# Performance work log

Measured on AMD Instinct MI355X. Metric: run time of the kernel, lower is better.

Reference implementation:

```python
import jax, jax.numpy as jnp
import numpy as np

N, E, De, Dv = 40000, 8000, 32, 8   # nodes, hyperedges, edge degree, node degree
D, Q, EIG, VOC, NC = 256, 256, 64, 1000, 40  # vertex/edge dim, query dim, eig dim, centrality vocab, classes
LN_EPS = 1e-5


def _linear(x, W, b):
    return x @ W + b


def _layernorm(x, g, b):
    mu = jnp.mean(x, axis=-1, keepdims=True)
    var = jnp.mean(jnp.square(x - mu), axis=-1, keepdims=True)
    return (x - mu) * jax.lax.rsqrt(var + LN_EPS) * g + b


def setup_inputs() -> dict:
    key = jax.random.key(0)
    ks = iter(jax.random.split(key, 64))
    def nrm(shape, s=0.02):
        return (jax.random.normal(next(ks), shape, jnp.float32) * s).astype(jnp.float32)
    inp = {
        'vfeat': jax.random.normal(next(ks), (N, D), jnp.float32),
        'efeat': jax.random.normal(next(ks), (E, D), jnp.float32),
        'eign_vec': jax.random.normal(next(ks), (N, EIG), jnp.float32),
        'feat_v_gcn': jax.random.normal(next(ks), (N, D), jnp.float32),
        'cent1': jax.random.uniform(next(ks), (E, De), jnp.float32),
        'cent2': jax.random.uniform(next(ks), (N, Dv), jnp.float32),
        'cent_idx': jax.random.randint(next(ks), (N,), 0, VOC),
        'uniq_idx': jax.random.randint(next(ks), (N,), 0, VOC),
        'edge2node': jax.random.randint(next(ks), (E, De), 0, N),
        'node2edge': jax.random.randint(next(ks), (N, Dv), 0, E),
        # learned parameters (W: [in, out])
        'W_vtx': nrm((D, D)), 'b_vtx': jnp.zeros((D,), jnp.float32),
        'W_pe': nrm((EIG, D)), 'b_pe': jnp.zeros((D,), jnp.float32),
        'cs_emb': nrm((VOC, D)), 'un_emb': nrm((VOC, D)),
        'W_kv': nrm((D, Q)), 'b_kv': jnp.zeros((Q,), jnp.float32),
        'W_vv': nrm((D, D)), 'b_vv': jnp.zeros((D,), jnp.float32),
        'W_qe': nrm((D, Q)), 'b_qe': jnp.zeros((Q,), jnp.float32),
        'W_ke': nrm((D, Q)), 'b_ke': jnp.zeros((Q,), jnp.float32),
        'W_ve': nrm((D, D)), 'b_ve': jnp.zeros((D,), jnp.float32),
        'W_qv': nrm((D, Q)), 'b_qv': jnp.zeros((Q,), jnp.float32),
        'W_l1': nrm((D, Q)), 'b_l1': jnp.zeros((Q,), jnp.float32),
        'W_l2': nrm((Q, D)), 'b_l2': jnp.zeros((D,), jnp.float32),
        'W_l3': nrm((D, Q)), 'b_l3': jnp.zeros((Q,), jnp.float32),
        'W_l4': nrm((Q, D)), 'b_l4': jnp.zeros((D,), jnp.float32),
        'ln1_g': jnp.ones((D,), jnp.float32), 'ln1_b': jnp.zeros((D,), jnp.float32),
        'ln2_g': jnp.ones((D,), jnp.float32), 'ln2_b': jnp.zeros((D,), jnp.float32),
        'W_cls': nrm((D, NC)), 'b_cls': jnp.zeros((NC,), jnp.float32),
    }
    return inp


def _forward(vfeat, efeat, eign_vec, feat_v_gcn, cent1, cent2,
             W_vtx, b_vtx, W_pe, b_pe, cs_emb, un_emb,
             W_kv, b_kv, W_vv, b_vv, W_qe, b_qe, W_ke, b_ke, W_ve, b_ve, W_qv, b_qv,
             W_l1, b_l1, W_l2, b_l2, W_l3, b_l3, W_l4, b_l4,
             ln1_g, ln1_b, ln2_g, ln2_b, W_cls, b_cls,
             cent_idx, uniq_idx, edge2node, node2edge):
    scale = 1.0 / np.sqrt(float(W_kv.shape[1]))  # 1/sqrt(query_dim)
    # first_layer feature assembly: vtx_lin_1layer + PE + GCN + centrality/uniqueness embeddings
    feat_v = (_linear(vfeat, W_vtx, b_vtx) + _linear(eign_vec, W_pe, b_pe)
              + feat_v_gcn + cs_emb[cent_idx] + un_emb[uniq_idx])
    feat_e = efeat

    # ---- stage 1: hyperedges attend over member nodes ('in' etype) ----
    k_n = _linear(feat_v, W_kv, b_kv)              # [N,Q]
    v_n = _linear(feat_v, W_vv, b_vv)              # [N,D]
    q_e = _linear(feat_e, W_qe, b_qe)              # [E,Q]
    km = k_n[edge2node]                            # [E,De,Q]
    attn = jax.nn.leaky_relu(jnp.einsum('edq,eq->ed', km, q_e), 0.01) * scale
    score = jax.nn.softmax(attn + cent1, axis=1)   # centrality-biased softmax (k-core + clustering)
    h_e = jnp.einsum('ed,edc->ec', score, v_n[edge2node])  # [E,D]
    x_e = _layernorm(h_e + feat_e, ln1_g, ln1_b)
    f_e = _linear(jax.nn.relu(_linear(x_e, W_l1, b_l1)), W_l2, b_l2)
    feat_e = _layernorm(f_e + x_e, ln1_g, ln1_b)

    # ---- stage 2: nodes attend over incident hyperedges ('con' etype) ----
    k_e = _linear(feat_e, W_ke, b_ke)              # [E,Q]
    v_e = _linear(feat_e, W_ve, b_ve)              # [E,D]
    q_v = _linear(feat_v, W_qv, b_qv)              # [N,Q]
    km2 = k_e[node2edge]                           # [N,Dv,Q]
    attn2 = jax.nn.leaky_relu(jnp.einsum('ndq,nq->nd', km2, q_v), 0.01) * scale
    score2 = jax.nn.softmax(attn2 + cent2, axis=1)
    h_v = jnp.einsum('nd,ndc->nc', score2, v_e[node2edge])  # [N,D]
    x_v = _layernorm(h_v + feat_v, ln2_g, ln2_b)
    f_v = _linear(jax.nn.relu(_linear(x_v, W_l3, b_l3)), W_l4, b_l4)
    feat_v = _layernorm(f_v + x_v, ln2_g, ln2_b)

    # last_layer classification head (dropout is identity in eval)
    return _linear(feat_v, W_cls, b_cls)           # [N,NC]


def reference(vfeat, efeat, eign_vec, feat_v_gcn, cent1, cent2,
              cent_idx, uniq_idx, edge2node, node2edge,
              W_vtx, b_vtx, W_pe, b_pe, cs_emb, un_emb,
              W_kv, b_kv, W_vv, b_vv, W_qe, b_qe, W_ke, b_ke, W_ve, b_ve, W_qv, b_qv,
              W_l1, b_l1, W_l2, b_l2, W_l3, b_l3, W_l4, b_l4,
              ln1_g, ln1_b, ln2_g, ln2_b, W_cls, b_cls):
    return _forward(vfeat, efeat, eign_vec, feat_v_gcn, cent1, cent2,
                    W_vtx, b_vtx, W_pe, b_pe, cs_emb, un_emb,
                    W_kv, b_kv, W_vv, b_vv, W_qe, b_qe, W_ke, b_ke, W_ve, b_ve, W_qv, b_qv,
                    W_l1, b_l1, W_l2, b_l2, W_l3, b_l3, W_l4, b_l4,
                    ln1_g, ln1_b, ln2_g, ln2_b, W_cls, b_cls,
                    cent_idx, uniq_idx, edge2node, node2edge)
```

## Files before the change

### kernel.cpp

```cpp
#include <hip/hip_runtime.h>
#include <hip/hip_bf16.h>
#include <cstddef>

#define N_NODES 40000
#define N_EDGES 8000
#define DE 32
#define DV 8
#define DIM 256
#define QDIM 256
#define EIGD 64
#define NCLS 40
#define LN_EPS 1e-5f
#define ATT_SCALE 0.0625f

typedef unsigned short u16;
typedef unsigned int u32;
using i16x8 = __attribute__((ext_vector_type(8))) short;
using f32x4 = __attribute__((ext_vector_type(4))) float;

__device__ inline u16 f2b(float f) {
    union { float f; u32 u; } c; c.f = f;
    u32 u = c.u + 0x7FFF + ((c.u >> 16) & 1);
    return (u16)(u >> 16);
}
__device__ inline float b2f(u16 b) {
    union { u32 u; float f; } c; c.u = (u32)b << 16;
    return c.f;
}

__device__ inline void gload_lds16(const u16* g, u16* l) {
    __builtin_amdgcn_global_load_lds(
        (const __attribute__((address_space(1))) void*)g,
        (__attribute__((address_space(3))) void*)l, 16, 0, 0);
}

#define VMCNT12 asm volatile("s_waitcnt vmcnt(12)" ::: "memory")
#define VMCNT6  asm volatile("s_waitcnt vmcnt(6)" ::: "memory")
#define VMCNT5  asm volatile("s_waitcnt vmcnt(5)" ::: "memory")
#define VMCNT4  asm volatile("s_waitcnt vmcnt(4)" ::: "memory")
#define VMCNT0  asm volatile("s_waitcnt vmcnt(0)" ::: "memory")
#define LGKM0   asm volatile("s_waitcnt lgkmcnt(0)" ::: "memory")

__global__ __launch_bounds__(256) void prep_weights(
    const float* w0, const float* w1, const float* w2, const float* w3,
    const float* w4, const float* w5, const float* w6, const float* w7,
    const float* w8, const float* w9, const float* w10, const float* w11,
    const float* w12, u16* __restrict__ pool)
{
    const float* srcs[13] = {w0,w1,w2,w3,w4,w5,w6,w7,w8,w9,w10,w11,w12};
    const int Ks[13]  = {256,64,256,256,256,256,256,256,256,256,256,256,256};
    const int Nds[13] = {256,256,256,256,256,256,256,256,256,256,256,256,40};
    const int id = blockIdx.z;
    const float* W = srcs[id];
    u16* Wt = pool + (size_t)id * 65536;
    const int K = Ks[id], Nd = Nds[id];
    const int k0 = blockIdx.x * 32, n0 = blockIdx.y * 32;
    if (k0 >= K || n0 >= Nd) return;

    __shared__ float tile[32][33];
    const int x = threadIdx.x & 31, y4 = (threadIdx.x >> 5) * 4;
#pragma unroll
    for (int j = 0; j < 4; j++) {
        int k = k0 + y4 + j;
        tile[y4 + j][x] = (k < K && (n0 + x) < Nd) ? W[(size_t)k * Nd + n0 + x] : 0.f;
    }
    __syncthreads();
#pragma unroll
    for (int j = 0; j < 4; j++) {
        int n = n0 + y4 + j;
        if (n < Nd && (k0 + x) < K)
            Wt[(size_t)n * K + k0 + x] = f2b(tile[x][y4 + j]);
    }
}

#define MST 264
__global__ __launch_bounds__(256, 2) void asm_kvq(
    const float* __restrict__ vfeat, const float* __restrict__ eign,
    const u16* __restrict__ Wt_vtx, const u16* __restrict__ Wt_pe,
    const float* __restrict__ b_vtx, const float* __restrict__ b_pe,
    const float* __restrict__ gcn, const float* __restrict__ emb1,
    const float* __restrict__ emb2, const int* __restrict__ idx1,
    const int* __restrict__ idx2,
    const u16* __restrict__ Wt_kvq, const float* __restrict__ b_kv,
    const float* __restrict__ b_vv, const float* __restrict__ b_qv,
    u16* __restrict__ FVb, u16* __restrict__ KVQn)
{
    __shared__ __align__(16) u16 Asm[2][64 * 32];
    __shared__ __align__(16) u16 Bsm[2][256 * 32];
    __shared__ __align__(16) u16 Msm[64 * MST];
    const int t = threadIdx.x;
    const int lane = t & 63, w = t >> 6;
    const int row0 = blockIdx.x * 64;

    const int srow = lane >> 2;
    const int sblk = ((lane & 3) ^ ((lane >> 3) & 3)) * 8;
    const int fr = lane & 15, h = lane >> 4;
    const int rsw = (fr >> 1) & 3;

    f32x4 acc[4][4] = {};
    float4 fA[2][2];

    auto p1_issueB = [&](int kt) {
        const int buf = kt & 1;
        const int k0 = kt << 5;
        const bool tail = (k0 >= 256);
#pragma unroll
        for (int i = 0; i < 4; i++) {
            const int r = w * 64 + i * 16;
            const u16* gp = tail ? Wt_pe + (size_t)(r + srow) * 64 + (k0 - 256) + sblk
                                 : Wt_vtx + (size_t)(r + srow) * 256 + k0 + sblk;
            gload_lds16(gp, &Bsm[buf][r * 32]);
        }
    };
    auto p1_loadA = [&](int kt) {
        const int k0 = kt << 5;
        const bool tail = (k0 >= 256);
        const float* ap = tail
            ? eign + (size_t)(row0 + w * 16 + srow) * 64 + (k0 - 256) + sblk
            : vfeat + (size_t)(row0 + w * 16 + srow) * 256 + k0 + sblk;
        fA[kt & 1][0] = *(const float4*)ap;
        fA[kt & 1][1] = *(const float4*)(ap + 4);
    };
    auto p1_write = [&](int kt) {
        const int buf = kt & 1;
        float4 f0 = fA[buf][0], f1 = fA[buf][1];
        i16x8 v;
        v[0] = (short)f2b(f0.x); v[1] = (short)f2b(f0.y);
        v[2] = (short)f2b(f0.z); v[3] = (short)f2b(f0.w);
        v[4] = (short)f2b(f1.x); v[5] = (short)f2b(f1.y);
        v[6] = (short)f2b(f1.z); v[7] = (short)f2b(f1.w);
        *(i16x8*)&Asm[buf][(w * 16 + srow) * 32 + (lane & 3) * 8] = v;
    };

    p1_loadA(0); p1_issueB(0); p1_loadA(1); p1_write(0);
#pragma unroll
    for (int kt = 0; kt < 10; ++kt) {
        const int buf = kt & 1;
        if (kt + 1 < 10) p1_issueB(kt + 1);
        if (kt + 2 < 10) p1_loadA(kt + 2);
        if (kt + 1 < 10) p1_write(kt + 1);
        else { VMCNT0; }
        LGKM0;
        __builtin_amdgcn_s_barrier();

        i16x8 af[4], bfr[4];
#pragma unroll
        for (int m = 0; m < 4; m++)
            af[m] = *(const i16x8*)&Asm[buf][(m * 16 + fr) * 32 + (h ^ rsw) * 8];
#pragma unroll
        for (int n = 0; n < 4; n++)
            bfr[n] = *(const i16x8*)&Bsm[buf][(w * 64 + n * 16 + fr) * 32 + (h ^ rsw) * 8];
        LGKM0;
        __builtin_amdgcn_sched_barrier(0);
        __builtin_amdgcn_s_barrier();

#pragma unroll
        for (int m = 0; m < 4; m++)
#pragma unroll
            for (int n = 0; n < 4; n++)
                acc[m][n] = __builtin_amdgcn_mfma_f32_16x16x32_bf16(
                    af[m], bfr[n], acc[m][n], 0, 0, 0);
    }

#pragma unroll
    for (int m = 0; m < 4; m++)
#pragma unroll
        for (int j = 0; j < 4; j++) {
            const int row = m * 16 + h * 4 + j;
#pragma unroll
            for (int n = 0; n < 4; n++) {
                const int col = w * 64 + n * 16 + fr;
                float v = acc[m][n][j] + b_vtx[col] + b_pe[col];
                Msm[row * MST + col] = f2b(v);
                acc[m][n][j] = 0.f;
            }
        }
    __syncthreads();

    const float4* gcn4 = (const float4*)gcn;
    const float4* e1_4 = (const float4*)emb1;
    const float4* e2_4 = (const float4*)emb2;
    ushort4* FVb4 = (ushort4*)FVb;
#pragma unroll 4
    for (int it = 0; it < 16; ++it) {
        const int T = t + it * 256;
        const int row = T >> 6, cg = T & 63;
        const int grow = row0 + row;
        const int i1 = idx1[grow], i2 = idx2[grow];
        ushort4 mv = *(const ushort4*)&Msm[row * MST + cg * 4];
        float4 gv = gcn4[(size_t)grow * 64 + cg];
        float4 e1 = e1_4[(size_t)i1 * 64 + cg];
        float4 e2 = e2_4[(size_t)i2 * 64 + cg];
        ushort4 o;
        o.x = f2b(b2f(mv.x) + gv.x + e1.x + e2.x);
        o.y = f2b(b2f(mv.y) + gv.y + e1.y + e2.y);
        o.z = f2b(b2f(mv.z) + gv.z + e1.z + e2.z);
        o.w = f2b(b2f(mv.w) + gv.w + e1.w + e2.w);
        FVb4[(size_t)grow * 64 + cg] = o;
        *(ushort4*)&Msm[row * MST + cg * 4] = o;
    }
    __syncthreads();

    auto p2_issueB = [&](int buf, int kt, const u16* Wb) {
#pragma unroll
        for (int i = 0; i < 4; i++) {
            const int r = w * 64 + i * 16;
            gload_lds16(Wb + (size_t)(r + srow) * 256 + (kt << 5) + sblk,
                        &Bsm[buf][r * 32]);
        }
    };
#pragma unroll 1
    for (int c = 0; c < 3; ++c) {
        const u16* Wb = Wt_kvq + (size_t)c * 256 * 256;
        const float* bc = (c == 0) ? b_kv : ((c == 1) ? b_vv : b_qv);
#pragma unroll
        for (int m = 0; m < 4; m++)
#pragma unroll
            for (int n = 0; n < 4; n++)
                acc[m][n] = f32x4{0.f, 0.f, 0.f, 0.f};
        p2_issueB(0, 0, Wb);
#pragma unroll
        for (int kt = 0; kt < 8; ++kt) {
            const int buf = kt & 1;
            if (kt < 7) { p2_issueB(buf ^ 1, kt + 1, Wb); VMCNT4; }
            else { VMCNT0; }
            __builtin_amdgcn_s_barrier();

            i16x8 af[4], bfr[4];
#pragma unroll
            for (int m = 0; m < 4; m++)
                af[m] = *(const i16x8*)&Msm[(m * 16 + fr) * MST + (kt << 5) + h * 8];
#pragma unroll
            for (int n = 0; n < 4; n++)
                bfr[n] = *(const i16x8*)&Bsm[buf][(w * 64 + n * 16 + fr) * 32 + (h ^ rsw) * 8];
            LGKM0;
            __builtin_amdgcn_sched_barrier(0);
            __builtin_amdgcn_s_barrier();

#pragma unroll
            for (int m = 0; m < 4; m++)
#pragma unroll
                for (int n = 0; n < 4; n++)
                    acc[m][n] = __builtin_amdgcn_mfma_f32_16x16x32_bf16(
                        af[m], bfr[n], acc[m][n], 0, 0, 0);
        }
#pragma unroll
        for (int m = 0; m < 4; m++)
#pragma unroll
            for (int j = 0; j < 4; j++) {
                const int grow = row0 + m * 16 + h * 4 + j;
#pragma unroll
                for (int n = 0; n < 4; n++) {
                    const int gcol = w * 64 + n * 16 + fr;
                    KVQn[(size_t)grow * 768 + c * 256 + gcol] =
                        f2b(acc[m][n][j] + bc[gcol]);
                }
            }
    }
}

template <int EPI, int AMODE, int NT>
__global__ __launch_bounds__(256, 2) void gemmN(
    const void* __restrict__ Av, const u16* __restrict__ Wt,
    const float* __restrict__ bias0, const float* __restrict__ bias1,
    const float* __restrict__ bias2,
    void* __restrict__ Cv, int Nd)
{
    __shared__ u16 Asm[3][64 * 64];
    __shared__ u16 Bsm[3][128 * 64];
    const int t = threadIdx.x;
    const int lane = t & 63, w = t >> 6;
    const int wr = w >> 1, wc = w & 1;
    const int row0 = blockIdx.y * 64, col0 = blockIdx.x * 128;

    f32x4 acc[2][4] = {};

    const int srow = lane >> 3;
    const int sblk = ((lane & 7) ^ srow) * 8;
    const int fr = lane & 15, h = lane >> 4;
    const int lsw = fr & 7;

    float4 farA[2][2][2];

    auto stage_load = [&](int kt) {
        const int buf = kt % 3;
        const int k0 = kt << 6;
        if constexpr (AMODE == 0) {
#pragma unroll
            for (int i = 0; i < 2; i++) {
                const int r = w * 16 + i * 8;
                gload_lds16((const u16*)Av + (size_t)(row0 + r + srow) * 256 + k0 + sblk,
                            &Asm[buf][r * 64]);
            }
        } else {
#pragma unroll
            for (int i = 0; i < 2; i++) {
                const int r = w * 16 + i * 8;
                const float* ap = (const float*)Av + (size_t)(row0 + r + srow) * 256 + k0 + sblk;
                farA[kt & 1][i][0] = *(const float4*)ap;
                farA[kt & 1][i][1] = *(const float4*)(ap + 4);
            }
        }
#pragma unroll
        for (int i = 0; i < 4; i++) {
            const int r = w * 32 + i * 8;
            int ng = col0 + r + srow; if (ng > Nd - 1) ng = Nd - 1;
            gload_lds16(Wt + (size_t)ng * 256 + k0 + sblk, &Bsm[buf][r * 64]);
        }
    };
    auto stage_write = [&](int kt) {
        const int buf = kt % 3;
#pragma unroll
        for (int i = 0; i < 2; i++) {
            const int r = w * 16 + i * 8;
            float4 f0 = farA[kt & 1][i][0], f1 = farA[kt & 1][i][1];
            i16x8 v;
            v[0] = (short)f2b(f0.x); v[1] = (short)f2b(f0.y);
            v[2] = (short)f2b(f0.z); v[3] = (short)f2b(f0.w);
            v[4] = (short)f2b(f1.x); v[5] = (short)f2b(f1.y);
            v[6] = (short)f2b(f1.z); v[7] = (short)f2b(f1.w);
            *(i16x8*)&Asm[buf][(r + srow) * 64 + (lane & 7) * 8] = v;
        }
    };

    stage_load(0);
    if (NT > 1) stage_load(1);
    if constexpr (AMODE != 0) stage_write(0);

#pragma unroll
    for (int kt = 0; kt < NT; ++kt) {
        const int buf = kt % 3;
        if (kt + 2 < NT) stage_load(kt + 2);
        if constexpr (AMODE != 0) {
            if (kt + 1 < NT) stage_write(kt + 1);
            else { VMCNT0; }
        } else {
            if (kt + 2 < NT) { VMCNT12; }
            else if (kt + 1 < NT) { VMCNT6; }
            else { VMCNT0; }
        }
        LGKM0;
        __builtin_amdgcn_s_barrier();

        i16x8 af[2][2], bfr[2][4];
#pragma unroll
        for (int kk = 0; kk < 2; kk++) {
#pragma unroll
            for (int m = 0; m < 2; m++)
                af[kk][m] = *(const i16x8*)&Asm[buf][(wr * 32 + m * 16 + fr) * 64 +
                                                    ((kk * 4 + h) ^ lsw) * 8];
#pragma unroll
            for (int n = 0; n < 4; n++)
                bfr[kk][n] = *(const i16x8*)&Bsm[buf][(wc * 64 + n * 16 + fr) * 64 +
                                                     ((kk * 4 + h) ^ lsw) * 8];
        }
        LGKM0;
        __builtin_amdgcn_sched_barrier(0);
        __builtin_amdgcn_s_barrier();

#pragma unroll
        for (int kk = 0; kk < 2; kk++)
#pragma unroll
            for (int m = 0; m < 2; m++)
#pragma unroll
                for (int n = 0; n < 4; n++)
                    acc[m][n] = __builtin_amdgcn_mfma_f32_16x16x32_bf16(
                        af[kk][m], bfr[kk][n], acc[m][n], 0, 0, 0);
    }

    const int seg = (int)(blockIdx.x >> 1);
    const float* bp = (seg == 0) ? bias0 : ((seg == 1) ? bias1 : bias2);
#pragma unroll
    for (int m = 0; m < 2; m++) {
#pragma unroll
        for (int j = 0; j < 4; j++) {
            const int grow = row0 + wr * 32 + m * 16 + h * 4 + j;
#pragma unroll
            for (int n = 0; n < 4; n++) {
                const int gcol = col0 + wc * 64 + n * 16 + fr;
                if (EPI == 4 && gcol >= Nd) continue;
                float v = acc[m][n][j] + bp[gcol & 255];
                if constexpr (EPI == 1) v = fmaxf(v, 0.f);
                if constexpr (EPI == 4)
                    ((float*)Cv)[(size_t)grow * Nd + gcol] = v;
                else
                    ((u16*)Cv)[(size_t)grow * Nd + gcol] = f2b(v);
            }
        }
    }
}

template <int TAIL>
__global__ __launch_bounds__(256, 2) void ffn_fused(
    const u16* __restrict__ X, const u16* __restrict__ Wt1,
    const float* __restrict__ b1, const u16* __restrict__ Wt2,
    const float* __restrict__ b2, const float* __restrict__ lng,
    const float* __restrict__ lnb, const u16* __restrict__ WtT,
    const float* __restrict__ bT0, const float* __restrict__ bT1,
    void* __restrict__ outp)
{
    __shared__ __align__(16) u16 Asm[2][64 * 32];
    __shared__ __align__(16) u16 Bsm[2][256 * 32];
    __shared__ __align__(16) u16 Msm[64 * MST];
    const int t = threadIdx.x;
    const int lane = t & 63, w = t >> 6;
    const int row0 = blockIdx.x * 64;

    const int srow = lane >> 2;
    const int sblk = ((lane & 3) ^ ((lane >> 3) & 3)) * 8;
    const int fr = lane & 15, h = lane >> 4;
    const int rsw = (fr >> 1) & 3;

    f32x4 acc[4][4] = {};

    auto stageA = [&](int buf, int kt) {
        gload_lds16(X + (size_t)(row0 + w * 16 + srow) * 256 + (kt << 5) + sblk,
                    &Asm[buf][(w * 16) * 32]);
    };
    auto stageB = [&](int buf, int kt, const u16* W) {
#pragma unroll
        for (int i = 0; i < 4; i++) {
            const int r = w * 64 + i * 16;
            gload_lds16(W + (size_t)(r + srow) * 256 + (kt << 5) + sblk,
                        &Bsm[buf][r * 32]);
        }
    };

    stageA(0, 0); stageB(0, 0, Wt1);
#pragma unroll
    for (int kt = 0; kt < 8; ++kt) {
        const int buf = kt & 1;
        if (kt < 7) { stageA(buf ^ 1, kt + 1); stageB(buf ^ 1, kt + 1, Wt1); VMCNT5; }
        else { VMCNT0; }
        __builtin_amdgcn_s_barrier();

        i16x8 af[4], bfr[4];
#pragma unroll
        for (int m = 0; m < 4; m++)
            af[m] = *(const i16x8*)&Asm[buf][(m * 16 + fr) * 32 + (h ^ rsw) * 8];
#pragma unroll
        for (int n = 0; n < 4; n++)
            bfr[n] = *(const i16x8*)&Bsm[buf][(w * 64 + n * 16 + fr) * 32 + (h ^ rsw) * 8];
        LGKM0;
        __builtin_amdgcn_sched_barrier(0);
        __builtin_amdgcn_s_barrier();

#pragma unroll
        for (int m = 0; m < 4; m++)
#pragma unroll
            for (int n = 0; n < 4; n++)
                acc[m][n] = __builtin_amdgcn_mfma_f32_16x16x32_bf16(
                    af[m], bfr[n], acc[m][n], 0, 0, 0);
    }
    {
        float b1v[4];
#pragma unroll
        for (int n = 0; n < 4; n++) b1v[n] = b1[w * 64 + n * 16 + fr];
#pragma unroll
        for (int m = 0; m < 4; m++)
#pragma unroll
            for (int j = 0; j < 4; j++) {
                const int row = m * 16 + h * 4 + j;
#pragma unroll
                for (int n = 0; n < 4; n++) {
                    const int col = w * 64 + n * 16 + fr;
                    float v = fmaxf(acc[m][n][j] + b1v[n], 0.f);
                    Msm[row * MST + col] = f2b(v);
                    acc[m][n][j] = 0.f;
                }
            }
    }
    __syncthreads();

    stageB(0, 0, Wt2);
#pragma unroll
    for (int kt = 0; kt < 8; ++kt) {
        const int buf = kt & 1;
        if (kt < 7) { stageB(buf ^ 1, kt + 1, Wt2); VMCNT4; }
        else { VMCNT0; }
        __builtin_amdgcn_s_barrier();

        i16x8 af[4], bfr[4];
#pragma unroll
        for (int m = 0; m < 4; m++)
            af[m] = *(const i16x8*)&Msm[(m * 16 + fr) * MST + (kt << 5) + h * 8];
#pragma unroll
        for (int n = 0; n < 4; n++)
            bfr[n] = *(const i16x8*)&Bsm[buf][(w * 64 + n * 16 + fr) * 32 + (h ^ rsw) * 8];
        LGKM0;
        __builtin_amdgcn_sched_barrier(0);
        __builtin_amdgcn_s_barrier();

#pragma unroll
        for (int m = 0; m < 4; m++)
#pragma unroll
            for (int n = 0; n < 4; n++)
                acc[m][n] = __builtin_amdgcn_mfma_f32_16x16x32_bf16(
                    af[m], bfr[n], acc[m][n], 0, 0, 0);
    }
    {
        float* redS = (float*)&Asm[0][0];
        float* redQ = redS + 256;
#pragma unroll
        for (int m = 0; m < 4; m++) {
#pragma unroll
            for (int j = 0; j < 4; j++) {
                const int grow = row0 + m * 16 + h * 4 + j;
                float s = 0.f, q = 0.f;
#pragma unroll
                for (int n = 0; n < 4; n++) {
                    const int gcol = w * 64 + n * 16 + fr;
                    float v = acc[m][n][j] + b2[gcol] +
                              b2f(X[(size_t)grow * 256 + gcol]);
                    acc[m][n][j] = v;
                    s += v; q += v * v;
                }
#pragma unroll
                for (int off = 1; off < 16; off <<= 1) {
                    s += __shfl_xor(s, off, 64);
                    q += __shfl_xor(q, off, 64);
                }
                if (fr == 0) {
                    redS[(m * 16 + h * 4 + j) * 4 + w] = s;
                    redQ[(m * 16 + h * 4 + j) * 4 + w] = q;
                }
            }
        }
        __syncthreads();
#pragma unroll
        for (int m = 0; m < 4; m++) {
#pragma unroll
            for (int j = 0; j < 4; j++) {
                const int r = m * 16 + h * 4 + j;
                float4 s4 = *(const float4*)&redS[r * 4];
                float4 q4 = *(const float4*)&redQ[r * 4];
                float mu = (s4.x + s4.y + s4.z + s4.w) * (1.f / DIM);
                float var = (q4.x + q4.y + q4.z + q4.w) * (1.f / DIM) - mu * mu;
                float rr = rsqrtf(var + LN_EPS);
#pragma unroll
                for (int n = 0; n < 4; n++) {
                    const int gcol = w * 64 + n * 16 + fr;
                    float y = (acc[m][n][j] - mu) * rr * lng[gcol] + lnb[gcol];
                    acc[m][n][j] = y;
                }
            }
        }
        __syncthreads();
#pragma unroll
        for (int m = 0; m < 4; m++)
#pragma unroll
            for (int j = 0; j < 4; j++) {
                const int row = m * 16 + h * 4 + j;
#pragma unroll
                for (int n = 0; n < 4; n++)
                    Msm[row * MST + (w * 64 + n * 16 + fr)] = f2b(acc[m][n][j]);
            }
    }
    VMCNT0;
    __syncthreads();

    if constexpr (TAIL == 0) {
        u16* KVe = (u16*)outp;
#pragma unroll
        for (int half = 0; half < 2; half++) {
            const u16* Wb = WtT + (size_t)half * 256 * 256;
            const float* bT = half ? bT1 : bT0;
#pragma unroll
            for (int m = 0; m < 4; m++)
#pragma unroll
                for (int n = 0; n < 4; n++)
                    acc[m][n] = f32x4{0.f, 0.f, 0.f, 0.f};
            stageB(0, 0, Wb);
#pragma unroll
            for (int kt = 0; kt < 8; ++kt) {
                const int buf = kt & 1;
                if (kt < 7) { stageB(buf ^ 1, kt + 1, Wb); VMCNT4; }
                else { VMCNT0; }
                __builtin_amdgcn_s_barrier();

                i16x8 af[4], bfr[4];
#pragma unroll
                for (int m = 0; m < 4; m++)
                    af[m] = *(const i16x8*)&Msm[(m * 16 + fr) * MST + (kt << 5) + h * 8];
#pragma unroll
                for (int n = 0; n < 4; n++)
                    bfr[n] = *(const i16x8*)&Bsm[buf][(w * 64 + n * 16 + fr) * 32 + (h ^ rsw) * 8];
                LGKM0;
                __builtin_amdgcn_sched_barrier(0);
                __builtin_amdgcn_s_barrier();

#pragma unroll
                for (int m = 0; m < 4; m++)
#pragma unroll
                    for (int n = 0; n < 4; n++)
                        acc[m][n] = __builtin_amdgcn_mfma_f32_16x16x32_bf16(
                            af[m], bfr[n], acc[m][n], 0, 0, 0);
            }
#pragma unroll
            for (int m = 0; m < 4; m++)
#pragma unroll
                for (int j = 0; j < 4; j++) {
                    const int grow = row0 + m * 16 + h * 4 + j;
#pragma unroll
                    for (int n = 0; n < 4; n++) {
                        const int gcol = w * 64 + n * 16 + fr;
                        KVe[(size_t)grow * 512 + half * 256 + gcol] =
                            f2b(acc[m][n][j] + bT[gcol]);
                    }
                }
        }
    } else {
        float* out = (float*)outp;
        f32x4 acc3[3] = {};
#pragma unroll
        for (int kk = 0; kk < 8; kk++) {
            i16x8 af = *(const i16x8*)&Msm[(w * 16 + fr) * MST + kk * 32 + h * 8];
#pragma unroll
            for (int n = 0; n < 3; n++) {
                int br = n * 16 + fr; if (br > NCLS - 1) br = NCLS - 1;
                i16x8 bfr = *(const i16x8*)(WtT + (size_t)br * 256 + kk * 32 + h * 8);
                acc3[n] = __builtin_amdgcn_mfma_f32_16x16x32_bf16(af, bfr, acc3[n], 0, 0, 0);
            }
        }
#pragma unroll
        for (int n = 0; n < 3; n++) {
            const int gcol = n * 16 + fr;
            if (gcol >= NCLS) continue;
#pragma unroll
            for (int j = 0; j < 4; j++) {
                const int grow = row0 + w * 16 + h * 4 + j;
                out[(size_t)grow * NCLS + gcol] = acc3[n][j] + bT0[gcol];
            }
        }
    }
}

__global__ __launch_bounds__(256) void edge_attn(
    const u16* __restrict__ KVQn, const u16* __restrict__ QE,
    const float* __restrict__ efeat,
    const int* __restrict__ e2n, const float* __restrict__ cent1,
    const float* __restrict__ g, const float* __restrict__ bb,
    u16* __restrict__ XE)
{
    const int lane = threadIdx.x & 63, w = threadIdx.x >> 6;
    const int e = blockIdx.x * 4 + w;
    const int c4 = lane * 4;

    ushort4 q4 = *(const ushort4*)&QE[(size_t)e * QDIM + c4];
    const float q0 = b2f(q4.x), q1 = b2f(q4.y), q2 = b2f(q4.z), q3 = b2f(q4.w);

    int4 rv[8];
#pragma unroll
    for (int i = 0; i < 8; i++)
        rv[i] = *(const int4*)&e2n[(size_t)e * DE + i * 4];
    int rows[DE];
#pragma unroll
    for (int i = 0; i < 8; i++) {
        rows[i * 4 + 0] = rv[i].x; rows[i * 4 + 1] = rv[i].y;
        rows[i * 4 + 2] = rv[i].z; rows[i * 4 + 3] = rv[i].w;
    }

    float p[DE];
#pragma unroll
    for (int g0 = 0; g0 < DE; g0 += 16) {
        ushort4 k4[16];
#pragma unroll
        for (int j = 0; j < 16; j++)
            k4[j] = *(const ushort4*)&KVQn[(size_t)rows[g0 + j] * 768 + c4];
#pragma unroll
        for (int j = 0; j < 16; j++)
            p[g0 + j] = q0 * b2f(k4[j].x) + q1 * b2f(k4[j].y)
                      + q2 * b2f(k4[j].z) + q3 * b2f(k4[j].w);
    }
#pragma unroll
    for (int off = 32; off; off >>= 1)
#pragma unroll
        for (int d = 0; d < DE; d++)
            p[d] += __shfl_xor(p[d], off, 64);

    float4 cv[8];
#pragma unroll
    for (int i = 0; i < 8; i++)
        cv[i] = *(const float4*)&cent1[(size_t)e * DE + i * 4];
    float cent[DE];
#pragma unroll
    for (int i = 0; i < 8; i++) {
        cent[i * 4 + 0] = cv[i].x; cent[i * 4 + 1] = cv[i].y;
        cent[i * 4 + 2] = cv[i].z; cent[i * 4 + 3] = cv[i].w;
    }
#pragma unroll
    for (int d = 0; d < DE; d++)
        p[d] = (p[d] > 0.f ? p[d] : 0.01f * p[d]) * ATT_SCALE + cent[d];

    float mx = p[0];
#pragma unroll
    for (int d = 1; d < DE; d++) mx = fmaxf(mx, p[d]);
    float s = 0.f;
#pragma unroll
    for (int d = 0; d < DE; d++) { p[d] = __expf(p[d] - mx); s += p[d]; }
    const float inv = 1.f / s;
#pragma unroll
    for (int d = 0; d < DE; d++) p[d] *= inv;

    float a0 = 0.f, a1 = 0.f, a2 = 0.f, a3 = 0.f;
#pragma unroll
    for (int g0 = 0; g0 < DE; g0 += 16) {
        ushort4 v4[16];
#pragma unroll
        for (int j = 0; j < 16; j++)
            v4[j] = *(const ushort4*)&KVQn[(size_t)rows[g0 + j] * 768 + 256 + c4];
#pragma unroll
        for (int j = 0; j < 16; j++) {
            const float sd = p[g0 + j];
            a0 = fmaf(sd, b2f(v4[j].x), a0); a1 = fmaf(sd, b2f(v4[j].y), a1);
            a2 = fmaf(sd, b2f(v4[j].z), a2); a3 = fmaf(sd, b2f(v4[j].w), a3);
        }
    }
    float4 ef = *(const float4*)&efeat[(size_t)e * DIM + c4];
    float x0 = a0 + ef.x, x1 = a1 + ef.y, x2 = a2 + ef.z, x3 = a3 + ef.w;

    float mu = x0 + x1 + x2 + x3;
#pragma unroll
    for (int off = 32; off; off >>= 1) mu += __shfl_xor(mu, off, 64);
    mu *= (1.f / DIM);
    float d0 = x0 - mu, d1 = x1 - mu, d2 = x2 - mu, d3 = x3 - mu;
    float var = d0 * d0 + d1 * d1 + d2 * d2 + d3 * d3;
#pragma unroll
    for (int off = 32; off; off >>= 1) var += __shfl_xor(var, off, 64);
    var *= (1.f / DIM);
    float r = rsqrtf(var + LN_EPS);
    float4 gv = *(const float4*)&g[c4];
    float4 bv = *(const float4*)&bb[c4];
    ushort4 o;
    o.x = f2b(d0 * r * gv.x + bv.x); o.y = f2b(d1 * r * gv.y + bv.y);
    o.z = f2b(d2 * r * gv.z + bv.z); o.w = f2b(d3 * r * gv.w + bv.w);
    *(ushort4*)&XE[(size_t)e * DIM + c4] = o;
}

__global__ __launch_bounds__(256) void node_attn(
    const u16* __restrict__ KVe, const u16* __restrict__ KVQn,
    const u16* __restrict__ FV,
    const int* __restrict__ n2e, const float* __restrict__ cent2,
    const float* __restrict__ g, const float* __restrict__ bb,
    u16* __restrict__ XV)
{
    const int lane = threadIdx.x & 63, w = threadIdx.x >> 6;
    const int na = blockIdx.x * 8 + w * 2, nb = na + 1;
    const int c4 = lane * 4;

    ushort4 qa4 = *(const ushort4*)&KVQn[(size_t)na * 768 + 512 + c4];
    ushort4 qb4 = *(const ushort4*)&KVQn[(size_t)nb * 768 + 512 + c4];
    const float qa0 = b2f(qa4.x), qa1 = b2f(qa4.y), qa2 = b2f(qa4.z), qa3 = b2f(qa4.w);
    const float qb0 = b2f(qb4.x), qb1 = b2f(qb4.y), qb2 = b2f(qb4.z), qb3 = b2f(qb4.w);

    int4 r0 = *(const int4*)&n2e[(size_t)na * DV];
    int4 r1 = *(const int4*)&n2e[(size_t)na * DV + 4];
    int4 r2 = *(const int4*)&n2e[(size_t)nb * DV];
    int4 r3 = *(const int4*)&n2e[(size_t)nb * DV + 4];
    int rA[8] = {r0.x, r0.y, r0.z, r0.w, r1.x, r1.y, r1.z, r1.w};
    int rB[8] = {r2.x, r2.y, r2.z, r2.w, r3.x, r3.y, r3.z, r3.w};

    ushort4 kA[8], vA[8], kB[8], vB[8];
#pragma unroll
    for (int d = 0; d < DV; d++) {
        const u16* b = KVe + (size_t)rA[d] * 512 + c4;
        kA[d] = *(const ushort4*)b; vA[d] = *(const ushort4*)(b + 256);
    }
#pragma unroll
    for (int d = 0; d < DV; d++) {
        const u16* b = KVe + (size_t)rB[d] * 512 + c4;
        kB[d] = *(const ushort4*)b; vB[d] = *(const ushort4*)(b + 256);
    }

    float pA[8], pB[8];
#pragma unroll
    for (int d = 0; d < DV; d++) {
        pA[d] = qa0 * b2f(kA[d].x) + qa1 * b2f(kA[d].y)
              + qa2 * b2f(kA[d].z) + qa3 * b2f(kA[d].w);
        pB[d] = qb0 * b2f(kB[d].x) + qb1 * b2f(kB[d].y)
              + qb2 * b2f(kB[d].z) + qb3 * b2f(kB[d].w);
    }
#pragma unroll
    for (int off = 32; off; off >>= 1) {
#pragma unroll
        for (int d = 0; d < DV; d++) {
            pA[d] += __shfl_xor(pA[d], off, 64);
            pB[d] += __shfl_xor(pB[d], off, 64);
        }
    }
    float4 cA0 = *(const float4*)&cent2[(size_t)na * DV];
    float4 cA1 = *(const float4*)&cent2[(size_t)na * DV + 4];
    float4 cB0 = *(const float4*)&cent2[(size_t)nb * DV];
    float4 cB1 = *(const float4*)&cent2[(size_t)nb * DV + 4];
    float cA[8] = {cA0.x, cA0.y, cA0.z, cA0.w, cA1.x, cA1.y, cA1.z, cA1.w};
    float cB[8] = {cB0.x, cB0.y, cB0.z, cB0.w, cB1.x, cB1.y, cB1.z, cB1.w};
#pragma unroll
    for (int d = 0; d < DV; d++) {
        pA[d] = (pA[d] > 0.f ? pA[d] : 0.01f * pA[d]) * ATT_SCALE + cA[d];
        pB[d] = (pB[d] > 0.f ? pB[d] : 0.01f * pB[d]) * ATT_SCALE + cB[d];
    }
    float mA = pA[0], mB = pB[0];
#pragma unroll
    for (int d = 1; d < DV; d++) { mA = fmaxf(mA, pA[d]); mB = fmaxf(mB, pB[d]); }
    float sA = 0.f, sB = 0.f;
#pragma unroll
    for (int d = 0; d < DV; d++) {
        pA[d] = __expf(pA[d] - mA); sA += pA[d];
        pB[d] = __expf(pB[d] - mB); sB += pB[d];
    }
    const float iA = 1.f / sA, iB = 1.f / sB;

    float a0 = 0.f, a1 = 0.f, a2 = 0.f, a3 = 0.f;
    float b0 = 0.f, b1 = 0.f, b2 = 0.f, b3 = 0.f;
#pragma unroll
    for (int d = 0; d < DV; d++) {
        const float sa = pA[d] * iA, sb = pB[d] * iB;
        a0 = fmaf(sa, b2f(vA[d].x), a0); a1 = fmaf(sa, b2f(vA[d].y), a1);
        a2 = fmaf(sa, b2f(vA[d].z), a2); a3 = fmaf(sa, b2f(vA[d].w), a3);
        b0 = fmaf(sb, b2f(vB[d].x), b0); b1 = fmaf(sb, b2f(vB[d].y), b1);
        b2 = fmaf(sb, b2f(vB[d].z), b2); b3 = fmaf(sb, b2f(vB[d].w), b3);
    }
    ushort4 fa = *(const ushort4*)&FV[(size_t)na * DIM + c4];
    ushort4 fb = *(const ushort4*)&FV[(size_t)nb * DIM + c4];
    float xa0 = a0 + b2f(fa.x), xa1 = a1 + b2f(fa.y);
    float xa2 = a2 + b2f(fa.z), xa3 = a3 + b2f(fa.w);
    float xb0 = b0 + b2f(fb.x), xb1 = b1 + b2f(fb.y);
    float xb2 = b2 + b2f(fb.z), xb3 = b3 + b2f(fb.w);

    float muA = xa0 + xa1 + xa2 + xa3, muB = xb0 + xb1 + xb2 + xb3;
#pragma unroll
    for (int off = 32; off; off >>= 1) {
        muA += __shfl_xor(muA, off, 64);
        muB += __shfl_xor(muB, off, 64);
    }
    muA *= (1.f / DIM); muB *= (1.f / DIM);
    float da0 = xa0 - muA, da1 = xa1 - muA, da2 = xa2 - muA, da3 = xa3 - muA;
    float db0 = xb0 - muB, db1 = xb1 - muB, db2 = xb2 - muB, db3 = xb3 - muB;
    float vA_ = da0 * da0 + da1 * da1 + da2 * da2 + da3 * da3;
    float vB_ = db0 * db0 + db1 * db1 + db2 * db2 + db3 * db3;
#pragma unroll
    for (int off = 32; off; off >>= 1) {
        vA_ += __shfl_xor(vA_, off, 64);
        vB_ += __shfl_xor(vB_, off, 64);
    }
    const float rA_ = rsqrtf(vA_ * (1.f / DIM) + LN_EPS);
    const float rB_ = rsqrtf(vB_ * (1.f / DIM) + LN_EPS);
    float4 gv = *(const float4*)&g[c4];
    float4 bv = *(const float4*)&bb[c4];
    ushort4 oa, ob;
    oa.x = f2b(da0 * rA_ * gv.x + bv.x); oa.y = f2b(da1 * rA_ * gv.y + bv.y);
    oa.z = f2b(da2 * rA_ * gv.z + bv.z); oa.w = f2b(da3 * rA_ * gv.w + bv.w);
    ob.x = f2b(db0 * rB_ * gv.x + bv.x); ob.y = f2b(db1 * rB_ * gv.y + bv.y);
    ob.z = f2b(db2 * rB_ * gv.z + bv.z); ob.w = f2b(db3 * rB_ * gv.w + bv.w);
    *(ushort4*)&XV[(size_t)na * DIM + c4] = oa;
    *(ushort4*)&XV[(size_t)nb * DIM + c4] = ob;
}

extern "C" void kernel_launch(void* const* d_in, const int* in_sizes, int n_in,
                              void* d_out, int out_size, void* d_ws, size_t ws_size,
                              hipStream_t stream)
{
    const float* vfeat  = (const float*)d_in[0];
    const float* efeat  = (const float*)d_in[1];
    const float* eign   = (const float*)d_in[2];
    const float* gcn    = (const float*)d_in[3];
    const float* cent1  = (const float*)d_in[4];
    const float* cent2  = (const float*)d_in[5];
    const int*   cidx   = (const int*)d_in[6];
    const int*   uidx   = (const int*)d_in[7];
    const int*   e2n    = (const int*)d_in[8];
    const int*   n2e    = (const int*)d_in[9];
    const float* W_vtx  = (const float*)d_in[10]; const float* b_vtx = (const float*)d_in[11];
    const float* W_pe   = (const float*)d_in[12]; const float* b_pe  = (const float*)d_in[13];
    const float* cs_emb = (const float*)d_in[14]; const float* un_emb= (const float*)d_in[15];
    const float* W_kv   = (const float*)d_in[16]; const float* b_kv  = (const float*)d_in[17];
    const float* W_vv   = (const float*)d_in[18]; const float* b_vv  = (const float*)d_in[19];
    const float* W_qe   = (const float*)d_in[20]; const float* b_qe  = (const float*)d_in[21];
    const float* W_ke   = (const float*)d_in[22]; const float* b_ke  = (const float*)d_in[23];
    const float* W_ve   = (const float*)d_in[24]; const float* b_ve  = (const float*)d_in[25];
    const float* W_qv   = (const float*)d_in[26]; const float* b_qv  = (const float*)d_in[27];
    const float* W_l1   = (const float*)d_in[28]; const float* b_l1  = (const float*)d_in[29];
    const float* W_l2   = (const float*)d_in[30]; const float* b_l2  = (const float*)d_in[31];
    const float* W_l3   = (const float*)d_in[32]; const float* b_l3  = (const float*)d_in[33];
    const float* W_l4   = (const float*)d_in[34]; const float* b_l4  = (const float*)d_in[35];
    const float* ln1_g  = (const float*)d_in[36]; const float* ln1_b = (const float*)d_in[37];
    const float* ln2_g  = (const float*)d_in[38]; const float* ln2_b = (const float*)d_in[39];
    const float* W_cls  = (const float*)d_in[40]; const float* b_cls = (const float*)d_in[41];
    float* out = (float*)d_out;

    const size_t NE = (size_t)N_NODES * DIM;
    const size_t EE = (size_t)N_EDGES * DIM;
    u16* ws = (u16*)d_ws;
    u16* FVb  = ws;
    u16* KVQn = FVb + NE;
    u16* B2   = KVQn + 3 * NE;
    u16* QEb  = B2 + NE;
    u16* XE   = QEb + EE;
    u16* KVe  = XE + EE;
    u16* Wp   = KVe + 2 * EE;
    u16* Wt_vtx = Wp +  0 * 65536;
    u16* Wt_pe  = Wp +  1 * 65536;
    u16* Wt_kvq = Wp +  2 * 65536;
    u16* Wt_qe  = Wp +  5 * 65536;
    u16* Wt_kve = Wp +  6 * 65536;
    u16* Wt_l1  = Wp +  8 * 65536;
    u16* Wt_l2  = Wp +  9 * 65536;
    u16* Wt_l3  = Wp + 10 * 65536;
    u16* Wt_l4  = Wp + 11 * 65536;
    u16* Wt_cls = Wp + 12 * 65536;

    const dim3 blk(256);
    const dim3 gW(8, 8, 13);
    const dim3 gQE(2, N_EDGES / 64);

    prep_weights<<<gW, blk, 0, stream>>>(
        W_vtx, W_pe, W_kv, W_vv, W_qv, W_qe, W_ke, W_ve,
        W_l1, W_l2, W_l3, W_l4, W_cls, Wp);

    asm_kvq<<<N_NODES / 64, blk, 0, stream>>>(
        vfeat, eign, Wt_vtx, Wt_pe, b_vtx, b_pe,
        gcn, cs_emb, un_emb, cidx, uidx,
        Wt_kvq, b_kv, b_vv, b_qv, FVb, KVQn);

    gemmN<0, 1, 4><<<gQE, blk, 0, stream>>>(efeat, Wt_qe,
        b_qe, b_qe, b_qe, QEb, 256);
    edge_attn<<<N_EDGES / 4, blk, 0, stream>>>(KVQn, QEb, efeat, e2n, cent1,
        ln1_g, ln1_b, XE);
    ffn_fused<0><<<N_EDGES / 64, blk, 0, stream>>>(XE, Wt_l1, b_l1,
        Wt_l2, b_l2, ln1_g, ln1_b, Wt_kve, b_ke, b_ve, KVe);

    node_attn<<<N_NODES / 8, blk, 0, stream>>>(KVe, KVQn, FVb, n2e, cent2,
        ln2_g, ln2_b, B2);
    ffn_fused<1><<<N_NODES / 64, blk, 0, stream>>>(B2, Wt_l3, b_l3,
        Wt_l4, b_l4, ln2_g, ln2_b, Wt_cls, b_cls, nullptr, out);
}
```

Measured before the change: 237.3 us.

## Restructure LDS double-buffer pipeline to one barrier per k-step and prefetch across GEMMs

The double-buffered weight staging loops now issue the next tile's loads before the MFMA block and wait for them with a single vmcnt(0) plus barrier after compute, replacing the previous wait-then-barrier and second barrier before compute. The first tile of each following GEMM (next weight chunk, the second FFN weight, the tail weights) is prefetched during the last k-step of the current one, so there is no cold load between chained GEMMs. The aim is fewer barriers per iteration and overlap of global-to-LDS copies with MFMA work. The cost is a full vmcnt(0) drain each step and tighter reliance on barrier placement to avoid overwriting buffers still being read.

```diff
diff --git a/kernel.cpp b/kernel.cpp
--- a/kernel.cpp
+++ b/kernel.cpp
@@ -36,10 +36,10 @@
 
 #define VMCNT12 asm volatile("s_waitcnt vmcnt(12)" ::: "memory")
 #define VMCNT6  asm volatile("s_waitcnt vmcnt(6)" ::: "memory")
-#define VMCNT5  asm volatile("s_waitcnt vmcnt(5)" ::: "memory")
-#define VMCNT4  asm volatile("s_waitcnt vmcnt(4)" ::: "memory")
 #define VMCNT0  asm volatile("s_waitcnt vmcnt(0)" ::: "memory")
 #define LGKM0   asm volatile("s_waitcnt lgkmcnt(0)" ::: "memory")
+#define SCHED0  __builtin_amdgcn_sched_barrier(0)
+#define SBAR    __builtin_amdgcn_s_barrier()
 
 __global__ __launch_bounds__(256) void prep_weights(
     const float* w0, const float* w1, const float* w2, const float* w3,
@@ -141,7 +141,7 @@
         if (kt + 1 < 10) p1_write(kt + 1);
         else { VMCNT0; }
         LGKM0;
-        __builtin_amdgcn_s_barrier();
+        SBAR;
 
         i16x8 af[4], bfr[4];
 #pragma unroll
@@ -151,8 +151,8 @@
         for (int n = 0; n < 4; n++)
             bfr[n] = *(const i16x8*)&Bsm[buf][(w * 64 + n * 16 + fr) * 32 + (h ^ rsw) * 8];
         LGKM0;
-        __builtin_amdgcn_sched_barrier(0);
-        __builtin_amdgcn_s_barrier();
+        SCHED0;
+        SBAR;
 
 #pragma unroll
         for (int m = 0; m < 4; m++)
@@ -209,22 +209,22 @@
                         &Bsm[buf][r * 32]);
         }
     };
+    p2_issueB(0, 0, Wt_kvq);
+    VMCNT0; SBAR;
 #pragma unroll 1
     for (int c = 0; c < 3; ++c) {
-        const u16* Wb = Wt_kvq + (size_t)c * 256 * 256;
+        const u16* Wb = Wt_kvq + (size_t)c * 65536;
         const float* bc = (c == 0) ? b_kv : ((c == 1) ? b_vv : b_qv);
 #pragma unroll
         for (int m = 0; m < 4; m++)
 #pragma unroll
             for (int n = 0; n < 4; n++)
                 acc[m][n] = f32x4{0.f, 0.f, 0.f, 0.f};
-        p2_issueB(0, 0, Wb);
 #pragma unroll
         for (int kt = 0; kt < 8; ++kt) {
             const int buf = kt & 1;
-            if (kt < 7) { p2_issueB(buf ^ 1, kt + 1, Wb); VMCNT4; }
-            else { VMCNT0; }
-            __builtin_amdgcn_s_barrier();
+            if (kt < 7) p2_issueB(buf ^ 1, kt + 1, Wb);
+            else if (c < 2) p2_issueB(0, 0, Wb + 65536);
 
             i16x8 af[4], bfr[4];
 #pragma unroll
@@ -234,15 +234,14 @@
             for (int n = 0; n < 4; n++)
                 bfr[n] = *(const i16x8*)&Bsm[buf][(w * 64 + n * 16 + fr) * 32 + (h ^ rsw) * 8];
             LGKM0;
-            __builtin_amdgcn_sched_barrier(0);
-            __builtin_amdgcn_s_barrier();
-
+            SCHED0;
 #pragma unroll
             for (int m = 0; m < 4; m++)
 #pragma unroll
                 for (int n = 0; n < 4; n++)
                     acc[m][n] = __builtin_amdgcn_mfma_f32_16x16x32_bf16(
                         af[m], bfr[n], acc[m][n], 0, 0, 0);
+            if (kt < 7) { VMCNT0; SBAR; }
         }
 #pragma unroll
         for (int m = 0; m < 4; m++)
@@ -256,6 +255,7 @@
                         f2b(acc[m][n][j] + bc[gcol]);
                 }
             }
+        if (c < 2) { VMCNT0; SBAR; }
     }
 }
 
@@ -340,7 +340,7 @@
             else { VMCNT0; }
         }
         LGKM0;
-        __builtin_amdgcn_s_barrier();
+        SBAR;
 
         i16x8 af[2][2], bfr[2][4];
 #pragma unroll
@@ -355,8 +355,8 @@
                                                      ((kk * 4 + h) ^ lsw) * 8];
         }
         LGKM0;
-        __builtin_amdgcn_sched_barrier(0);
-        __builtin_amdgcn_s_barrier();
+        SCHED0;
+        SBAR;
 
 #pragma unroll
         for (int kk = 0; kk < 2; kk++)
@@ -427,12 +427,12 @@
     };
 
     stageA(0, 0); stageB(0, 0, Wt1);
+    VMCNT0; SBAR;
 #pragma unroll
     for (int kt = 0; kt < 8; ++kt) {
         const int buf = kt & 1;
-        if (kt < 7) { stageA(buf ^ 1, kt + 1); stageB(buf ^ 1, kt + 1, Wt1); VMCNT5; }
-        else { VMCNT0; }
-        __builtin_amdgcn_s_barrier();
+        if (kt < 7) { stageA(buf ^ 1, kt + 1); stageB(buf ^ 1, kt + 1, Wt1); }
+        else        { stageB(0, 0, Wt2); }
 
         i16x8 af[4], bfr[4];
 #pragma unroll
@@ -442,15 +442,14 @@
         for (int n = 0; n < 4; n++)
             bfr[n] = *(const i16x8*)&Bsm[buf][(w * 64 + n * 16 + fr) * 32 + (h ^ rsw) * 8];
         LGKM0;
-        __builtin_amdgcn_sched_barrier(0);
-        __builtin_amdgcn_s_barrier();
-
+        SCHED0;
 #pragma unroll
         for (int m = 0; m < 4; m++)
 #pragma unroll
             for (int n = 0; n < 4; n++)
                 acc[m][n] = __builtin_amdgcn_mfma_f32_16x16x32_bf16(
                     af[m], bfr[n], acc[m][n], 0, 0, 0);
+        if (kt < 7) { VMCNT0; SBAR; }
     }
     {
         float b1v[4];
@@ -472,13 +471,11 @@
     }
     __syncthreads();
 
-    stageB(0, 0, Wt2);
 #pragma unroll
     for (int kt = 0; kt < 8; ++kt) {
         const int buf = kt & 1;
-        if (kt < 7) { stageB(buf ^ 1, kt + 1, Wt2); VMCNT4; }
-        else { VMCNT0; }
-        __builtin_amdgcn_s_barrier();
+        if (kt < 7) stageB(buf ^ 1, kt + 1, Wt2);
+        else if (TAIL == 0) stageB(0, 0, WtT);
 
         i16x8 af[4], bfr[4];
 #pragma unroll
@@ -488,15 +485,14 @@
         for (int n = 0; n < 4; n++)
             bfr[n] = *(const i16x8*)&Bsm[buf][(w * 64 + n * 16 + fr) * 32 + (h ^ rsw) * 8];
         LGKM0;
-        __builtin_amdgcn_sched_barrier(0);
-        __builtin_amdgcn_s_barrier();
-
+        SCHED0;
 #pragma unroll
         for (int m = 0; m < 4; m++)
 #pragma unroll
             for (int n = 0; n < 4; n++)
                 acc[m][n] = __builtin_amdgcn_mfma_f32_16x16x32_bf16(
                     af[m], bfr[n], acc[m][n], 0, 0, 0);
+        if (kt < 7) { VMCNT0; SBAR; }
     }
     {
         float* redS = (float*)&Asm[0][0];
@@ -556,27 +552,24 @@
                     Msm[row * MST + (w * 64 + n * 16 + fr)] = f2b(acc[m][n][j]);
             }
     }
-    VMCNT0;
     __syncthreads();
 
     if constexpr (TAIL == 0) {
         u16* KVe = (u16*)outp;
-#pragma unroll
+#pragma unroll 1
         for (int half = 0; half < 2; half++) {
-            const u16* Wb = WtT + (size_t)half * 256 * 256;
+            const u16* Wb = WtT + (size_t)half * 65536;
             const float* bT = half ? bT1 : bT0;
 #pragma unroll
             for (int m = 0; m < 4; m++)
 #pragma unroll
                 for (int n = 0; n < 4; n++)
                     acc[m][n] = f32x4{0.f, 0.f, 0.f, 0.f};
-            stageB(0, 0, Wb);
 #pragma unroll
             for (int kt = 0; kt < 8; ++kt) {
                 const int buf = kt & 1;
-                if (kt < 7) { stageB(buf ^ 1, kt + 1, Wb); VMCNT4; }
-                else { VMCNT0; }
-                __builtin_amdgcn_s_barrier();
+                if (kt < 7) stageB(buf ^ 1, kt + 1, Wb);
+                else if (half == 0) stageB(0, 0, WtT + 65536);
 
                 i16x8 af[4], bfr[4];
 #pragma unroll
@@ -586,15 +579,14 @@
                 for (int n = 0; n < 4; n++)
                     bfr[n] = *(const i16x8*)&Bsm[buf][(w * 64 + n * 16 + fr) * 32 + (h ^ rsw) * 8];
                 LGKM0;
-                __builtin_amdgcn_sched_barrier(0);
-                __builtin_amdgcn_s_barrier();
-
+                SCHED0;
 #pragma unroll
                 for (int m = 0; m < 4; m++)
 #pragma unroll
                     for (int n = 0; n < 4; n++)
                         acc[m][n] = __builtin_amdgcn_mfma_f32_16x16x32_bf16(
                             af[m], bfr[n], acc[m][n], 0, 0, 0);
+                if (kt < 7) { VMCNT0; SBAR; }
             }
 #pragma unroll
             for (int m = 0; m < 4; m++)
@@ -608,6 +600,7 @@
                             f2b(acc[m][n][j] + bT[gcol]);
                     }
                 }
+            if (half == 0) { VMCNT0; SBAR; }
         }
     } else {
         float* out = (float*)outp;
```

Result: no change. 237.7 us (+0.2%).
